# Kernel tuning notes

Measured on AMD Instinct MI355X. Metric: run time of the kernel, lower is better.

The kernel has to match this reference:

```python
import jax, jax.numpy as jnp
import numpy as np

D_MODEL = 2048
N_HEADS = 16
HEAD_DIM = D_MODEL // N_HEADS  # 128
MAX_POS = 2048


def _precompute_cos_sin(max_pos, head_dim):
    inv_freq = 1.0 / (10000.0 ** (jnp.arange(0, head_dim, 2, dtype=jnp.float32) / head_dim))
    t = jnp.arange(max_pos, dtype=jnp.float32)
    freqs = jnp.outer(t, inv_freq)          # [max_pos, head_dim//2]
    emb = jnp.concatenate([freqs, freqs], axis=-1)  # [max_pos, head_dim]
    return jnp.cos(emb), jnp.sin(emb)


def _rotate_half(x):
    x1, x2 = x[..., : x.shape[-1] // 2], x[..., x.shape[-1] // 2 :]
    return jnp.concatenate([-x2, x1], axis=-1)


def setup_inputs() -> dict:
    key = jax.random.key(0)
    kx, kq, kk, kv, ko = jax.random.split(key, 5)
    B, S = 2, 2048
    x = jax.random.normal(kx, (B, S, D_MODEL), dtype=jnp.float32)
    scale = 1.0 / np.sqrt(D_MODEL)
    # torch Linear weights are [out_features, in_features]
    Wq = jax.random.normal(kq, (D_MODEL, D_MODEL), dtype=jnp.float32) * scale
    Wk = jax.random.normal(kk, (D_MODEL, D_MODEL), dtype=jnp.float32) * scale
    Wv = jax.random.normal(kv, (D_MODEL, D_MODEL), dtype=jnp.float32) * scale
    Wo = jax.random.normal(ko, (D_MODEL, D_MODEL), dtype=jnp.float32) * scale
    cos, sin = _precompute_cos_sin(MAX_POS, HEAD_DIM)
    # causal mask: True where attention is disallowed (masked_fill semantics)
    mask = jnp.triu(jnp.ones((S, S), dtype=bool), k=1)
    mask = jnp.broadcast_to(mask[None], (B, S, S))
    return {"x": x, "Wq": Wq, "Wk": Wk, "Wv": Wv, "Wo": Wo,
            "cos": cos, "sin": sin, "mask": mask}


def reference(x, Wq, Wk, Wv, Wo, cos, sin, mask):
    B, S, _ = x.shape
    H, Dh = N_HEADS, HEAD_DIM
    scaling = Dh ** -0.5

    def split_heads(y):  # [B,S,D] -> [B,H,S,Dh]
        return y.reshape(B, S, H, Dh).transpose(0, 2, 1, 3)

    q = split_heads(x @ Wq.T)
    k = split_heads(x @ Wk.T)
    v = split_heads(x @ Wv.T)

    c = cos[:S][None, None]  # [1,1,S,Dh]
    s = sin[:S][None, None]
    q = q * c + _rotate_half(q) * s
    k = k * c + _rotate_half(k) * s

    scores = jnp.einsum("bhqd,bhkd->bhqk", q, k) * scaling
    scores = jnp.where(mask[:, None], -jnp.inf, scores)
    attn = jax.nn.softmax(scores, axis=-1)
    out = jnp.einsum("bhqk,bhkd->bhqd", attn, v)  # [B,H,S,Dh]
    out = out.transpose(0, 2, 1, 3).reshape(B, S, H * Dh)
    return out @ Wo.T
```

## Files before the change

kernel.cpp:

```cpp
#include <hip/hip_runtime.h>

typedef float f32x4 __attribute__((ext_vector_type(4)));
typedef short s16x8 __attribute__((ext_vector_type(8)));
typedef unsigned short u16;
typedef u16 u16x4 __attribute__((ext_vector_type(4)));

#define SEQ 2048
#define BATCH 2
#define NH 16
#define DH 128
#define DM 2048
#define MROWS (BATCH * SEQ)

__device__ constexpr float SCALE2 = 0.12751879523531f;

__device__ __forceinline__ u16 f2bf(float f) {
  unsigned u = __float_as_uint(f);
  u += 0x7fffu + ((u >> 16) & 1u);
  return (u16)(u >> 16);
}
__device__ __forceinline__ float bf2f(u16 b) {
  return __uint_as_float(((unsigned)b) << 16);
}

__device__ __forceinline__ void gld_lds16(const void* g, void* l) {
  __builtin_amdgcn_global_load_lds(
      (const __attribute__((address_space(1))) unsigned int*)g,
      (__attribute__((address_space(3))) unsigned int*)l, 16, 0, 0);
}

__global__ __launch_bounds__(256) void cast_all(const float* __restrict__ x,
                                                const float* __restrict__ Wq,
                                                const float* __restrict__ Wk,
                                                const float* __restrict__ Wv,
                                                const float* __restrict__ Wo,
                                                u16* __restrict__ xb,
                                                u16* __restrict__ Wqkvb,
                                                u16* __restrict__ Wob) {
  long i = (long)blockIdx.x * 256 + threadIdx.x;
  const float* src;
  u16* dst;
  long off;
  if (i < 2097152)      { src = x;  dst = xb;              off = i; }
  else if (i < 3145728) { src = Wq; dst = Wqkvb;           off = i - 2097152; }
  else if (i < 4194304) { src = Wk; dst = Wqkvb + 4194304; off = i - 3145728; }
  else if (i < 5242880) { src = Wv; dst = Wqkvb + 8388608; off = i - 4194304; }
  else                  { src = Wo; dst = Wob;             off = i - 5242880; }
  float4 v = ((const float4*)src)[off];
  u16x4 o;
  o[0] = f2bf(v.x); o[1] = f2bf(v.y); o[2] = f2bf(v.z); o[3] = f2bf(v.w);
  ((u16x4*)dst)[off] = o;
}


#define GEMM_V3_BODY(A, B, NTILE_SHIFT)                                       \
  __shared__ u16 Alds[2][256 * 64];                                           \
  __shared__ u16 Blds[2][128 * 64];                                           \
  const int tid = threadIdx.x, wave = tid >> 6, lane = tid & 63;              \
  const int r = lane & 15, g = lane >> 4;                                     \
  const int wm = wave >> 1, wn = wave & 1;                                    \
  const int bid = blockIdx.x;                                                 \
  const int swz = (bid & 7) * (gridDim.x >> 3) + (bid >> 3);                  \
  const int m0 = (swz & 15) * 256;                                            \
  const int n0 = (swz >> 4) * 128;                                            \
  const int lrow = lane >> 3;                                                 \
  const int csrc = (lane & 7) ^ lrow;                                         \
  f32x4 acc[4][4] = {};                                                       \
  s16x8 aF[2][4], bF[2][4];                                                   \
  STAGE_A(0, 0, 0); STAGE_B(0, 0, 0); STAGE_A(0, 1, 0); STAGE_B(0, 1, 0);     \
  STAGE_A(1, 0, 1); STAGE_B(1, 0, 1);                                         \
  asm volatile("s_waitcnt vmcnt(3)" ::: "memory");                            \
  __builtin_amdgcn_s_barrier();                                               \
  for (int t = 0; t < 32; ++t) {                                              \
    const int bt = t & 1, bn = bt ^ 1;                                        \
    const u16* Ab = Alds[bt];                                                 \
    const u16* Bb = Blds[bt];                                                 \
    READ_K(0);                                                                \
    __builtin_amdgcn_sched_barrier(0);                                        \
    READ_K(1);                                                                \
    if (t < 31) { STAGE_A(t + 1, 1, bn); STAGE_B(t + 1, 1, bn); }             \
    asm volatile("s_waitcnt lgkmcnt(8)" ::: "memory");                        \
    __builtin_amdgcn_sched_barrier(0);                                        \
    MFMA_K(0);                                                                \
    asm volatile("s_waitcnt lgkmcnt(0)" ::: "memory");                        \
    __builtin_amdgcn_sched_barrier(0);                                        \
    __builtin_amdgcn_s_barrier();                                             \
    if (t < 30) { STAGE_A(t + 2, 0, bt); STAGE_B(t + 2, 0, bt); }             \
    MFMA_K(1);                                                                \
    if (t < 30)       asm volatile("s_waitcnt vmcnt(3)" ::: "memory");        \
    else if (t == 30) asm volatile("s_waitcnt vmcnt(0)" ::: "memory");        \
    __builtin_amdgcn_s_barrier();                                             \
  }

#define STAGE_A(TA, MH, BUF) do {                                             \
  _Pragma("unroll") for (int i_ = 0; i_ < 2; ++i_) {                          \
    const int row0_ = (MH) * 128 + i_ * 64 + wave * 8;                        \
    gld_lds16(A + (long)(m0 + row0_ + lrow) * 2048 + (TA) * 64 + csrc * 8,    \
              &Alds[BUF][row0_ * 64]);                                        \
  } } while (0)
#define STAGE_B(TA, NHh, BUF) do {                                            \
    const int row0_ = (NHh) * 64 + wave * 8;                                  \
    gld_lds16(B + (long)(n0 + row0_ + lrow) * 2048 + (TA) * 64 + csrc * 8,    \
              &Blds[BUF][row0_ * 64]);                                        \
  } while (0)
#define READ_K(KK) do {                                                       \
  _Pragma("unroll") for (int mf = 0; mf < 4; ++mf) {                          \
    const int arow = wm * 64 + mf * 16 + r;                                   \
    aF[KK][mf] = *(const s16x8*)&Ab[arow * 64 +                               \
                                    ((((KK) * 4 + g) ^ (arow & 7)) * 8)];     \
  }                                                                           \
  _Pragma("unroll") for (int nf = 0; nf < 4; ++nf) {                          \
    const int brow = wn * 64 + nf * 16 + r;                                   \
    bF[KK][nf] = *(const s16x8*)&Bb[brow * 64 +                               \
                                    ((((KK) * 4 + g) ^ (brow & 7)) * 8)];     \
  } } while (0)
#define MFMA_K(KK) do {                                                       \
  __builtin_amdgcn_s_setprio(1);                                              \
  _Pragma("unroll") for (int mf = 0; mf < 4; ++mf)                            \
    _Pragma("unroll") for (int nf = 0; nf < 4; ++nf)                          \
      acc[mf][nf] = __builtin_amdgcn_mfma_f32_16x16x32_bf16(                  \
          aF[KK][mf], bF[KK][nf], acc[mf][nf], 0, 0, 0);                      \
  __builtin_amdgcn_s_setprio(0);                                              \
} while (0)

__global__ __launch_bounds__(512, 2) void gemm_qkv8(const u16* __restrict__ A,
                                                    const u16* __restrict__ B,
                                                    u16* __restrict__ Qo,
                                                    u16* __restrict__ Ko,
                                                    u16* __restrict__ Vo) {
  GEMM_V3_BODY(A, B, 4)
  u16* Cb = (n0 < 2048) ? Qo : (n0 < 4096 ? Ko : Vo);
  const int nc0 = n0 & 2047;
#pragma unroll
  for (int mi = 0; mi < 4; ++mi)
#pragma unroll
    for (int ni = 0; ni < 4; ++ni)
#pragma unroll
      for (int q = 0; q < 4; ++q)
        Cb[(long)(m0 + wm * 64 + mi * 16 + g * 4 + q) * 2048 +
           nc0 + wn * 64 + ni * 16 + r] = f2bf(acc[mi][ni][q]);
}

__global__ __launch_bounds__(512, 2) void gemm_wo(const u16* __restrict__ A,
                                                  const u16* __restrict__ B,
                                                  float* __restrict__ C) {
  GEMM_V3_BODY(A, B, 4)
#pragma unroll
  for (int mi = 0; mi < 4; ++mi)
#pragma unroll
    for (int ni = 0; ni < 4; ++ni)
#pragma unroll
      for (int q = 0; q < 4; ++q)
        C[(long)(m0 + wm * 64 + mi * 16 + g * 4 + q) * 2048 +
          n0 + wn * 64 + ni * 16 + r] = acc[mi][ni][q];
}

#undef MFMA_K
#undef READ_K
#undef STAGE_B
#undef STAGE_A
#undef GEMM_V3_BODY

__global__ __launch_bounds__(256) void rope_kernel(u16* __restrict__ Q, u16* __restrict__ K,
                                                   const float* __restrict__ cosT,
                                                   const float* __restrict__ sinT) {
  int idx = blockIdx.x * 256 + threadIdx.x;
  int d = idx & 63;
  int h = (idx >> 6) & 15;
  int s = (idx >> 10) & 2047;
  int b = idx >> 21;
  float c = cosT[s * DH + d];
  float sn = sinT[s * DH + d];
  long base = ((long)(b * SEQ + s)) * DM + h * DH + d;
  float q1 = bf2f(Q[base]), q2 = bf2f(Q[base + 64]);
  Q[base]      = f2bf(q1 * c - q2 * sn);
  Q[base + 64] = f2bf(q2 * c + q1 * sn);
  float k1 = bf2f(K[base]), k2 = bf2f(K[base + 64]);
  K[base]      = f2bf(k1 * c - k2 * sn);
  K[base + 64] = f2bf(k2 * c + k1 * sn);
}

__global__ __launch_bounds__(256) void transpose_v(const u16* __restrict__ Vlin,
                                                   u16* __restrict__ Vt) {
  __shared__ u16 tile[64][129];
  int t = threadIdx.x;
  int st = blockIdx.x & 31;
  int h = (blockIdx.x >> 5) & 15;
  int b = blockIdx.x >> 9;
  int s0 = st * 64;
  const u16* src = Vlin + ((long)(b * SEQ + s0)) * DM + h * DH;
#pragma unroll
  for (int rr = 0; rr < 4; rr++) {
    int row = rr * 16 + (t >> 4);
    int col = (t & 15) * 8;
    s16x8 v = *(const s16x8*)&src[(long)row * DM + col];
#pragma unroll
    for (int j = 0; j < 8; j++) tile[row][col + j] = (u16)v[j];
  }
  __syncthreads();
  u16* dst = Vt + ((long)(b * NH + h)) * DH * SEQ + s0;
#pragma unroll
  for (int rr = 0; rr < 4; rr++) {
    int d = rr * 32 + (t >> 3);
    int sc = (t & 7) * 8;
    s16x8 o;
#pragma unroll
    for (int j = 0; j < 8; j++) o[j] = (short)tile[sc + j][d];
    *(s16x8*)&dst[(long)d * SEQ + sc] = o;
  }
}


__device__ __forceinline__ void softmax_swapped(
    f32x4 (&s)[4], float& mi, float& li,
    u16 (&pl)[16][64], float (&als)[16],
    int qbase, int k0, int r, int g) {
  const int q = qbase + r;
  const bool edge = (k0 + 63) > qbase;
  float v[16];
#pragma unroll
  for (int kk = 0; kk < 4; kk++)
#pragma unroll
    for (int i = 0; i < 4; i++) {
      float x = s[kk][i] * SCALE2;
      if (edge && (k0 + kk * 16 + g * 4 + i > q)) x = -1e30f;
      v[kk * 4 + i] = x;
    }
  float t8[8], t4[4];
#pragma unroll
  for (int j = 0; j < 8; j++) t8[j] = fmaxf(v[2 * j], v[2 * j + 1]);
#pragma unroll
  for (int j = 0; j < 4; j++) t4[j] = fmaxf(t8[2 * j], t8[2 * j + 1]);
  float mx = fmaxf(fmaxf(t4[0], t4[1]), fmaxf(t4[2], t4[3]));
  mx = fmaxf(mx, __shfl_xor(mx, 16, 64));
  mx = fmaxf(mx, __shfl_xor(mx, 32, 64));
  const float mnew = fmaxf(mi, mx);
  const float a = exp2f(mi - mnew);
  float p[16];
#pragma unroll
  for (int j = 0; j < 16; j++) p[j] = exp2f(v[j] - mnew);
  float s8[8], s4[4];
#pragma unroll
  for (int j = 0; j < 8; j++) s8[j] = p[2 * j] + p[2 * j + 1];
#pragma unroll
  for (int j = 0; j < 4; j++) s4[j] = s8[2 * j] + s8[2 * j + 1];
  float ps = (s4[0] + s4[1]) + (s4[2] + s4[3]);
  ps += __shfl_xor(ps, 16, 64);
  ps += __shfl_xor(ps, 32, 64);
  li = li * a + ps;
  mi = mnew;
  const int sw = (r & 7) << 3;
#pragma unroll
  for (int kk = 0; kk < 4; kk++) {
    u16x4 w;
#pragma unroll
    for (int i = 0; i < 4; i++) w[i] = f2bf(p[kk * 4 + i]);
    *(u16x4*)&pl[r][(kk * 16 + g * 4) ^ sw] = w;
  }
  als[r] = a;
}

__global__ __launch_bounds__(512, 4) void attn_kernel(const u16* __restrict__ Q,
                                                      const u16* __restrict__ K,
                                                      const u16* __restrict__ Vt,
                                                      u16* __restrict__ O) {
  __shared__ u16 Klds[64 * 128];
  __shared__ u16 Vlds[128 * 64];
  __shared__ u16 Plds[8][16][64];
  __shared__ float Alds[8][16];

  const int tid = threadIdx.x, wave = tid >> 6, lane = tid & 63;
  const int r = lane & 15, g = lane >> 4;
  const int bh = blockIdx.x & 31;
  const int jj = blockIdx.x >> 5;
  const int j = (jj < 8) ? jj : 23 - jj;
  const int h = bh & 15, b = bh >> 4;
  const bool isB = wave >= 4;
  const int w4 = wave & 3;
  const int strip = isB ? (31 - j) : j;
  const int q0 = strip * 64 + w4 * 16;
  const int nt = 32 - j;
  const int lastA = j;

  const u16* Qbh = Q + (long)b * SEQ * DM + h * DH;
  const u16* Kbh = K + (long)b * SEQ * DM + h * DH;
  const u16* Vbh = Vt + ((long)(b * NH + h)) * DH * SEQ;

  s16x8 qf[4];
#pragma unroll
  for (int jq = 0; jq < 4; jq++)
    qf[jq] = *(const s16x8*)&Qbh[(long)(q0 + r) * DM + jq * 32 + g * 8];

  f32x4 oacc[8] = {};
  float mi = -1e30f, li = 0.f;

  for (int kt = 0; kt < nt; ++kt) {
    const int k0 = kt * 64;
    __syncthreads();
#pragma unroll
    for (int c = 0; c < 2; ++c) {
      const int s = c * 512 + tid;
      const int krow = s >> 4;
      const int kch = (s & 15) ^ (krow & 7);
      gld_lds16(Kbh + (long)(k0 + krow) * DM + kch * 8,
                &Klds[(c * 512 + wave * 64) * 8]);
      const int vrow = s >> 3;
      const int vch = (s & 7) ^ (vrow & 7);
      gld_lds16(Vbh + (long)vrow * SEQ + k0 + vch * 8,
                &Vlds[(c * 512 + wave * 64) * 8]);
    }
    __syncthreads();

    const bool active = isB || (kt <= lastA);
    if (active) {
      f32x4 sacc[4] = {};
#pragma unroll
      for (int kk = 0; kk < 4; kk++) {
#pragma unroll
        for (int jq = 0; jq < 4; jq++) {
          s16x8 kf = *(const s16x8*)&Klds[(kk * 16 + r) * 128 +
                                          (((jq * 4 + g) ^ (r & 7)) * 8)];
          sacc[kk] = __builtin_amdgcn_mfma_f32_16x16x32_bf16(kf, qf[jq], sacc[kk], 0, 0, 0);
        }
      }
      softmax_swapped(sacc, mi, li, Plds[wave], Alds[wave], q0, k0, r, g);

      f32x4 av = *(const f32x4*)&Alds[wave][g * 4];
#pragma unroll
      for (int f = 0; f < 8; f++)
#pragma unroll
        for (int i = 0; i < 4; i++) oacc[f][i] *= av[i];

      const int sw = (r & 7) << 3;
#pragma unroll
      for (int kc = 0; kc < 2; kc++) {
        s16x8 pf = *(const s16x8*)&Plds[wave][r][(kc * 32 + g * 8) ^ sw];
#pragma unroll
        for (int f = 0; f < 8; f++) {
          s16x8 vf = *(const s16x8*)&Vlds[(f * 16 + r) * 64 +
                                          (((kc * 4 + g) ^ (r & 7)) * 8)];
          oacc[f] = __builtin_amdgcn_mfma_f32_16x16x32_bf16(pf, vf, oacc[f], 0, 0, 0);
        }
      }
    }
  }

  Alds[wave][r] = 1.f / li;
  f32x4 iv = *(const f32x4*)&Alds[wave][g * 4];
  u16* Obh = O + (long)b * SEQ * DM + h * DH;
#pragma unroll
  for (int f = 0; f < 8; f++)
#pragma unroll
    for (int i = 0; i < 4; i++)
      Obh[(long)(q0 + g * 4 + i) * DM + f * 16 + r] = f2bf(oacc[f][i] * iv[i]);
}

extern "C" void kernel_launch(void* const* d_in, const int* in_sizes, int n_in,
                              void* d_out, int out_size, void* d_ws, size_t ws_size,
                              hipStream_t stream) {
  const float* x    = (const float*)d_in[0];
  const float* Wq   = (const float*)d_in[1];
  const float* Wk   = (const float*)d_in[2];
  const float* Wv   = (const float*)d_in[3];
  const float* Wo   = (const float*)d_in[4];
  const float* cosT = (const float*)d_in[5];
  const float* sinT = (const float*)d_in[6];

  if (ws_size < (size_t)134217728) return;

  char* ws = (char*)d_ws;
  u16* xb    = (u16*)(ws);
  u16* Wqkvb = (u16*)(ws + 16777216);
  u16* Wob   = (u16*)(ws + 41943040);
  u16* Qlin  = (u16*)(ws + 50331648);
  u16* Klin  = (u16*)(ws + 67108864);
  u16* Vlin  = (u16*)(ws + 83886080);
  u16* Vt    = (u16*)(ws + 100663296);
  u16* Olin  = (u16*)(ws + 117440512);

  cast_all<<<24576, 256, 0, stream>>>(x, Wq, Wk, Wv, Wo, xb, Wqkvb, Wob);

  gemm_qkv8<<<768, 512, 0, stream>>>(xb, Wqkvb, Qlin, Klin, Vlin);

  rope_kernel<<<16384, 256, 0, stream>>>(Qlin, Klin, cosT, sinT);
  transpose_v<<<1024, 256, 0, stream>>>(Vlin, Vt);
  attn_kernel<<<512, 512, 0, stream>>>(Qlin, Klin, Vt, Olin);

  gemm_wo<<<256, 512, 0, stream>>>(Olin, Wob, (float*)d_out);
}
```

Before: 264.9 us.

## Fuse V transpose into QKV GEMM epilogue and give attention waves two query tiles

The QKV GEMM epilogue for V tiles now stages results in shared memory and writes them directly in transposed [b,h,d,s] layout, which removes the separate transpose_v kernel and the Vlin round trip. The attention kernel drops from 8 waves per block to 4, and each wave now processes two 16-row query tiles. This reuses each K and V fragment read from LDS across twice as many MFMAs. The trade-offs are fewer waves to hide latency, higher register pressure from doubled accumulators, and extra shared-memory synchronization in the GEMM epilogue.

```diff
diff --git a/kernel.cpp b/kernel.cpp
--- a/kernel.cpp
+++ b/kernel.cpp
@@ -53,7 +53,7 @@
 }
 
 
-#define GEMM_V3_BODY(A, B, NTILE_SHIFT)                                       \
+#define GEMM_V3_BODY(A, B)                                                    \
   __shared__ u16 Alds[2][256 * 64];                                           \
   __shared__ u16 Blds[2][128 * 64];                                           \
   const int tid = threadIdx.x, wave = tid >> 6, lane = tid & 63;              \
@@ -127,24 +127,50 @@
                                                     const u16* __restrict__ B,
                                                     u16* __restrict__ Qo,
                                                     u16* __restrict__ Ko,
-                                                    u16* __restrict__ Vo) {
-  GEMM_V3_BODY(A, B, 4)
-  u16* Cb = (n0 < 2048) ? Qo : (n0 < 4096 ? Ko : Vo);
-  const int nc0 = n0 & 2047;
-#pragma unroll
-  for (int mi = 0; mi < 4; ++mi)
-#pragma unroll
-    for (int ni = 0; ni < 4; ++ni)
-#pragma unroll
-      for (int q = 0; q < 4; ++q)
-        Cb[(long)(m0 + wm * 64 + mi * 16 + g * 4 + q) * 2048 +
-           nc0 + wn * 64 + ni * 16 + r] = f2bf(acc[mi][ni][q]);
+                                                    u16* __restrict__ Vt) {
+  GEMM_V3_BODY(A, B)
+  if (n0 < 4096) {
+    u16* Cb = (n0 < 2048) ? Qo : Ko;
+    const int nc0 = n0 & 2047;
+#pragma unroll
+    for (int mi = 0; mi < 4; ++mi)
+#pragma unroll
+      for (int ni = 0; ni < 4; ++ni)
+#pragma unroll
+        for (int q = 0; q < 4; ++q)
+          Cb[(long)(m0 + wm * 64 + mi * 16 + g * 4 + q) * 2048 +
+             nc0 + wn * 64 + ni * 16 + r] = f2bf(acc[mi][ni][q]);
+  } else {
+    u16* T = (u16*)Alds;
+#pragma unroll
+    for (int mi = 0; mi < 4; ++mi)
+#pragma unroll
+      for (int ni = 0; ni < 4; ++ni) {
+        const int d = wn * 64 + ni * 16 + r;
+        const int sb = wm * 64 + mi * 16 + g * 4;
+        u16x4 w;
+#pragma unroll
+        for (int q = 0; q < 4; ++q) w[q] = f2bf(acc[mi][ni][q]);
+        *(u16x4*)&T[d * 256 + (((sb >> 3) ^ (d & 7)) << 3) + (sb & 7)] = w;
+      }
+    __syncthreads();
+    const int b_ = m0 >> 11, s0l = m0 & 2047;
+    const int hh = (n0 - 4096) >> 7;
+    const int dd = tid >> 2, part = tid & 3;
+    u16* vrow = Vt + ((long)((b_ * 16 + hh) * 128 + dd)) * 2048 + s0l;
+#pragma unroll
+    for (int cc = 0; cc < 8; ++cc) {
+      const int chunk = cc * 4 + part;
+      s16x8 v = *(const s16x8*)&T[dd * 256 + ((chunk ^ (dd & 7)) << 3)];
+      *(s16x8*)&vrow[chunk * 8] = v;
+    }
+  }
 }
 
 __global__ __launch_bounds__(512, 2) void gemm_wo(const u16* __restrict__ A,
                                                   const u16* __restrict__ B,
                                                   float* __restrict__ C) {
-  GEMM_V3_BODY(A, B, 4)
+  GEMM_V3_BODY(A, B)
 #pragma unroll
   for (int mi = 0; mi < 4; ++mi)
 #pragma unroll
@@ -180,36 +206,6 @@
   K[base + 64] = f2bf(k2 * c + k1 * sn);
 }
 
-__global__ __launch_bounds__(256) void transpose_v(const u16* __restrict__ Vlin,
-                                                   u16* __restrict__ Vt) {
-  __shared__ u16 tile[64][129];
-  int t = threadIdx.x;
-  int st = blockIdx.x & 31;
-  int h = (blockIdx.x >> 5) & 15;
-  int b = blockIdx.x >> 9;
-  int s0 = st * 64;
-  const u16* src = Vlin + ((long)(b * SEQ + s0)) * DM + h * DH;
-#pragma unroll
-  for (int rr = 0; rr < 4; rr++) {
-    int row = rr * 16 + (t >> 4);
-    int col = (t & 15) * 8;
-    s16x8 v = *(const s16x8*)&src[(long)row * DM + col];
-#pragma unroll
-    for (int j = 0; j < 8; j++) tile[row][col + j] = (u16)v[j];
-  }
-  __syncthreads();
-  u16* dst = Vt + ((long)(b * NH + h)) * DH * SEQ + s0;
-#pragma unroll
-  for (int rr = 0; rr < 4; rr++) {
-    int d = rr * 32 + (t >> 3);
-    int sc = (t & 7) * 8;
-    s16x8 o;
-#pragma unroll
-    for (int j = 0; j < 8; j++) o[j] = (short)tile[sc + j][d];
-    *(s16x8*)&dst[(long)d * SEQ + sc] = o;
-  }
-}
-
 
 __device__ __forceinline__ void softmax_swapped(
     f32x4 (&s)[4], float& mi, float& li,
@@ -260,14 +256,14 @@
   als[r] = a;
 }
 
-__global__ __launch_bounds__(512, 4) void attn_kernel(const u16* __restrict__ Q,
+__global__ __launch_bounds__(256, 2) void attn_kernel(const u16* __restrict__ Q,
                                                       const u16* __restrict__ K,
                                                       const u16* __restrict__ Vt,
                                                       u16* __restrict__ O) {
   __shared__ u16 Klds[64 * 128];
   __shared__ u16 Vlds[128 * 64];
-  __shared__ u16 Plds[8][16][64];
-  __shared__ float Alds[8][16];
+  __shared__ u16 Plds[4][2][16][64];
+  __shared__ float Alds[4][2][16];
 
   const int tid = threadIdx.x, wave = tid >> 6, lane = tid & 63;
   const int r = lane & 15, g = lane >> 4;
@@ -275,10 +271,10 @@
   const int jj = blockIdx.x >> 5;
   const int j = (jj < 8) ? jj : 23 - jj;
   const int h = bh & 15, b = bh >> 4;
-  const bool isB = wave >= 4;
-  const int w4 = wave & 3;
+  const bool isB = wave >= 2;
+  const int w2 = wave & 1;
   const int strip = isB ? (31 - j) : j;
-  const int q0 = strip * 64 + w4 * 16;
+  const int q0 = strip * 64 + w2 * 32;
   const int nt = 32 - j;
   const int lastA = j;
 
@@ -286,73 +282,87 @@
   const u16* Kbh = K + (long)b * SEQ * DM + h * DH;
   const u16* Vbh = Vt + ((long)(b * NH + h)) * DH * SEQ;
 
-  s16x8 qf[4];
-#pragma unroll
-  for (int jq = 0; jq < 4; jq++)
-    qf[jq] = *(const s16x8*)&Qbh[(long)(q0 + r) * DM + jq * 32 + g * 8];
-
-  f32x4 oacc[8] = {};
-  float mi = -1e30f, li = 0.f;
+  s16x8 qfA[4], qfB[4];
+#pragma unroll
+  for (int jq = 0; jq < 4; jq++) {
+    qfA[jq] = *(const s16x8*)&Qbh[(long)(q0 + r) * DM + jq * 32 + g * 8];
+    qfB[jq] = *(const s16x8*)&Qbh[(long)(q0 + 16 + r) * DM + jq * 32 + g * 8];
+  }
+
+  f32x4 oaccA[8] = {}, oaccB[8] = {};
+  float miA = -1e30f, liA = 0.f, miB = -1e30f, liB = 0.f;
 
   for (int kt = 0; kt < nt; ++kt) {
     const int k0 = kt * 64;
     __syncthreads();
 #pragma unroll
-    for (int c = 0; c < 2; ++c) {
-      const int s = c * 512 + tid;
+    for (int c = 0; c < 4; ++c) {
+      const int s = c * 256 + tid;
       const int krow = s >> 4;
       const int kch = (s & 15) ^ (krow & 7);
       gld_lds16(Kbh + (long)(k0 + krow) * DM + kch * 8,
-                &Klds[(c * 512 + wave * 64) * 8]);
+                &Klds[(c * 256 + wave * 64) * 8]);
       const int vrow = s >> 3;
       const int vch = (s & 7) ^ (vrow & 7);
       gld_lds16(Vbh + (long)vrow * SEQ + k0 + vch * 8,
-                &Vlds[(c * 512 + wave * 64) * 8]);
+                &Vlds[(c * 256 + wave * 64) * 8]);
     }
     __syncthreads();
 
     const bool active = isB || (kt <= lastA);
     if (active) {
-      f32x4 sacc[4] = {};
+      f32x4 sA[4] = {}, sB[4] = {};
 #pragma unroll
       for (int kk = 0; kk < 4; kk++) {
 #pragma unroll
         for (int jq = 0; jq < 4; jq++) {
           s16x8 kf = *(const s16x8*)&Klds[(kk * 16 + r) * 128 +
                                           (((jq * 4 + g) ^ (r & 7)) * 8)];
-          sacc[kk] = __builtin_amdgcn_mfma_f32_16x16x32_bf16(kf, qf[jq], sacc[kk], 0, 0, 0);
+          sA[kk] = __builtin_amdgcn_mfma_f32_16x16x32_bf16(kf, qfA[jq], sA[kk], 0, 0, 0);
+          sB[kk] = __builtin_amdgcn_mfma_f32_16x16x32_bf16(kf, qfB[jq], sB[kk], 0, 0, 0);
         }
       }
-      softmax_swapped(sacc, mi, li, Plds[wave], Alds[wave], q0, k0, r, g);
-
-      f32x4 av = *(const f32x4*)&Alds[wave][g * 4];
+      softmax_swapped(sA, miA, liA, Plds[wave][0], Alds[wave][0], q0, k0, r, g);
+      softmax_swapped(sB, miB, liB, Plds[wave][1], Alds[wave][1], q0 + 16, k0, r, g);
+
+      f32x4 avA = *(const f32x4*)&Alds[wave][0][g * 4];
+      f32x4 avB = *(const f32x4*)&Alds[wave][1][g * 4];
 #pragma unroll
       for (int f = 0; f < 8; f++)
 #pragma unroll
-        for (int i = 0; i < 4; i++) oacc[f][i] *= av[i];
+        for (int i = 0; i < 4; i++) {
+          oaccA[f][i] *= avA[i];
+          oaccB[f][i] *= avB[i];
+        }
 
       const int sw = (r & 7) << 3;
 #pragma unroll
       for (int kc = 0; kc < 2; kc++) {
-        s16x8 pf = *(const s16x8*)&Plds[wave][r][(kc * 32 + g * 8) ^ sw];
+        s16x8 pfA = *(const s16x8*)&Plds[wave][0][r][(kc * 32 + g * 8) ^ sw];
+        s16x8 pfB = *(const s16x8*)&Plds[wave][1][r][(kc * 32 + g * 8) ^ sw];
 #pragma unroll
         for (int f = 0; f < 8; f++) {
           s16x8 vf = *(const s16x8*)&Vlds[(f * 16 + r) * 64 +
                                           (((kc * 4 + g) ^ (r & 7)) * 8)];
-          oacc[f] = __builtin_amdgcn_mfma_f32_16x16x32_bf16(pf, vf, oacc[f], 0, 0, 0);
+          oaccA[f] = __builtin_amdgcn_mfma_f32_16x16x32_bf16(pfA, vf, oaccA[f], 0, 0, 0);
+          oaccB[f] = __builtin_amdgcn_mfma_f32_16x16x32_bf16(pfB, vf, oaccB[f], 0, 0, 0);
         }
       }
     }
   }
 
-  Alds[wave][r] = 1.f / li;
-  f32x4 iv = *(const f32x4*)&Alds[wave][g * 4];
+  Alds[wave][0][r] = 1.f / liA;
+  Alds[wave][1][r] = 1.f / liB;
+  f32x4 ivA = *(const f32x4*)&Alds[wave][0][g * 4];
+  f32x4 ivB = *(const f32x4*)&Alds[wave][1][g * 4];
   u16* Obh = O + (long)b * SEQ * DM + h * DH;
 #pragma unroll
   for (int f = 0; f < 8; f++)
 #pragma unroll
-    for (int i = 0; i < 4; i++)
-      Obh[(long)(q0 + g * 4 + i) * DM + f * 16 + r] = f2bf(oacc[f][i] * iv[i]);
+    for (int i = 0; i < 4; i++) {
+      Obh[(long)(q0 + g * 4 + i) * DM + f * 16 + r] = f2bf(oaccA[f][i] * ivA[i]);
+      Obh[(long)(q0 + 16 + g * 4 + i) * DM + f * 16 + r] = f2bf(oaccB[f][i] * ivB[i]);
+    }
 }
 
 extern "C" void kernel_launch(void* const* d_in, const int* in_sizes, int n_in,
@@ -374,17 +384,15 @@
   u16* Wob   = (u16*)(ws + 41943040);
   u16* Qlin  = (u16*)(ws + 50331648);
   u16* Klin  = (u16*)(ws + 67108864);
-  u16* Vlin  = (u16*)(ws + 83886080);
   u16* Vt    = (u16*)(ws + 100663296);
   u16* Olin  = (u16*)(ws + 117440512);
 
   cast_all<<<24576, 256, 0, stream>>>(x, Wq, Wk, Wv, Wo, xb, Wqkvb, Wob);
 
-  gemm_qkv8<<<768, 512, 0, stream>>>(xb, Wqkvb, Qlin, Klin, Vlin);
+  gemm_qkv8<<<768, 512, 0, stream>>>(xb, Wqkvb, Qlin, Klin, Vt);
 
   rope_kernel<<<16384, 256, 0, stream>>>(Qlin, Klin, cosT, sinT);
-  transpose_v<<<1024, 256, 0, stream>>>(Vlin, Vt);
-  attn_kernel<<<512, 512, 0, stream>>>(Qlin, Klin, Vt, Olin);
+  attn_kernel<<<512, 256, 0, stream>>>(Qlin, Klin, Vt, Olin);
 
   gemm_wo<<<256, 512, 0, stream>>>(Olin, Wob, (float*)d_out);
 }
```

Result: slower. 270.9 us (+2.3%).

## Fuse RoPE and V transpose into QKV GEMM epilogue via LDS staging

Applied to the files above, without the earlier changes.

The QKV GEMM epilogue now stages each output tile through shared memory. For Q and K tiles it applies rotary embedding using the partner half-dimension before writing. For V tiles it writes directly in the transposed per-head layout the attention kernel expects. This removes the separate rope and transpose kernels along with their extra global read/write passes, at the cost of an extra LDS round trip, a barrier and per-element cos/sin loads in the GEMM epilogue.

```diff
diff --git a/kernel.cpp b/kernel.cpp
--- a/kernel.cpp
+++ b/kernel.cpp
@@ -53,9 +53,10 @@
 }
 
 
-#define GEMM_V3_BODY(A, B, NTILE_SHIFT)                                       \
-  __shared__ u16 Alds[2][256 * 64];                                           \
-  __shared__ u16 Blds[2][128 * 64];                                           \
+#define GEMM_V3_BODY(A, B)                                                    \
+  __shared__ u16 SMEM[49152];                                      \
+  u16 (*Alds)[16384] = (u16(*)[16384])SMEM;                    \
+  u16 (*Blds)[8192]  = (u16(*)[8192])(SMEM + 32768);           \
   const int tid = threadIdx.x, wave = tid >> 6, lane = tid & 63;              \
   const int r = lane & 15, g = lane >> 4;                                     \
   const int wm = wave >> 1, wn = wave & 1;                                    \
@@ -125,26 +126,76 @@
 
 __global__ __launch_bounds__(512, 2) void gemm_qkv8(const u16* __restrict__ A,
                                                     const u16* __restrict__ B,
+                                                    const float* __restrict__ cosT,
+                                                    const float* __restrict__ sinT,
                                                     u16* __restrict__ Qo,
                                                     u16* __restrict__ Ko,
-                                                    u16* __restrict__ Vo) {
-  GEMM_V3_BODY(A, B, 4)
-  u16* Cb = (n0 < 2048) ? Qo : (n0 < 4096 ? Ko : Vo);
-  const int nc0 = n0 & 2047;
-#pragma unroll
-  for (int mi = 0; mi < 4; ++mi)
-#pragma unroll
-    for (int ni = 0; ni < 4; ++ni)
-#pragma unroll
-      for (int q = 0; q < 4; ++q)
-        Cb[(long)(m0 + wm * 64 + mi * 16 + g * 4 + q) * 2048 +
-           nc0 + wn * 64 + ni * 16 + r] = f2bf(acc[mi][ni][q]);
+                                                    u16* __restrict__ Vt) {
+  GEMM_V3_BODY(A, B)
+  if (n0 < 4096) {
+    u16* T = SMEM;
+#pragma unroll
+    for (int mi = 0; mi < 4; ++mi)
+#pragma unroll
+      for (int ni = 0; ni < 4; ++ni) {
+        const int rl = wm * 64 + mi * 16 + g * 4;
+        const int dh = wn * 64 + ni * 16 + r;
+#pragma unroll
+        for (int q = 0; q < 4; ++q)
+          T[(rl + q) * 136 + dh] = f2bf(acc[mi][ni][q]);
+      }
+    __syncthreads();
+    u16* Cb = (n0 < 2048) ? Qo : Ko;
+    const int nc0 = n0 & 2047;
+    const float sgn = wn ? 1.f : -1.f;
+#pragma unroll
+    for (int mi = 0; mi < 4; ++mi)
+#pragma unroll
+      for (int ni = 0; ni < 4; ++ni) {
+        const int rl = wm * 64 + mi * 16 + g * 4;
+        const int dh = wn * 64 + ni * 16 + r;
+#pragma unroll
+        for (int q = 0; q < 4; ++q) {
+          const int row = m0 + rl + q;
+          const int spos = row & 2047;
+          const float c  = cosT[spos * 128 + dh];
+          const float sn = sinT[spos * 128 + dh];
+          const float v = bf2f(T[(rl + q) * 136 + dh]);
+          const float p = bf2f(T[(rl + q) * 136 + (dh ^ 64)]);
+          Cb[(long)row * 2048 + nc0 + dh] = f2bf(v * c + sgn * p * sn);
+        }
+      }
+  } else {
+    u16* T = SMEM;
+#pragma unroll
+    for (int mi = 0; mi < 4; ++mi)
+#pragma unroll
+      for (int ni = 0; ni < 4; ++ni) {
+        const int d = wn * 64 + ni * 16 + r;
+        const int sb = wm * 64 + mi * 16 + g * 4;
+        u16x4 w;
+#pragma unroll
+        for (int q = 0; q < 4; ++q) w[q] = f2bf(acc[mi][ni][q]);
+        *(u16x4*)&T[d * 256 + (((sb >> 3) ^ (d & 7)) << 3) + (sb & 7)] = w;
+      }
+    __syncthreads();
+    const int b_ = m0 >> 11, s0l = m0 & 2047;
+    const int hh = (n0 - 4096) >> 7;
+    const int dd = tid >> 2, part = tid & 3;
+    u16* vrow = Vt + ((long)((b_ * 16 + hh) * 128 + dd)) * 2048 + s0l;
+#pragma unroll
+    for (int cc = 0; cc < 8; ++cc) {
+      const int chunk = cc * 4 + part;
+      s16x8 v = *(const s16x8*)&T[dd * 256 + ((chunk ^ (dd & 7)) << 3)];
+      *(s16x8*)&vrow[chunk * 8] = v;
+    }
+  }
 }
 
 __global__ __launch_bounds__(512, 2) void gemm_wo(const u16* __restrict__ A,
                                                   const u16* __restrict__ B,
                                                   float* __restrict__ C) {
-  GEMM_V3_BODY(A, B, 4)
+  GEMM_V3_BODY(A, B)
 #pragma unroll
   for (int mi = 0; mi < 4; ++mi)
 #pragma unroll
@@ -160,55 +211,6 @@
 #undef STAGE_B
 #undef STAGE_A
 #undef GEMM_V3_BODY
-
-__global__ __launch_bounds__(256) void rope_kernel(u16* __restrict__ Q, u16* __restrict__ K,
-                                                   const float* __restrict__ cosT,
-                                                   const float* __restrict__ sinT) {
-  int idx = blockIdx.x * 256 + threadIdx.x;
-  int d = idx & 63;
-  int h = (idx >> 6) & 15;
-  int s = (idx >> 10) & 2047;
-  int b = idx >> 21;
-  float c = cosT[s * DH + d];
-  float sn = sinT[s * DH + d];
-  long base = ((long)(b * SEQ + s)) * DM + h * DH + d;
-  float q1 = bf2f(Q[base]), q2 = bf2f(Q[base + 64]);
-  Q[base]      = f2bf(q1 * c - q2 * sn);
-  Q[base + 64] = f2bf(q2 * c + q1 * sn);
-  float k1 = bf2f(K[base]), k2 = bf2f(K[base + 64]);
-  K[base]      = f2bf(k1 * c - k2 * sn);
-  K[base + 64] = f2bf(k2 * c + k1 * sn);
-}
-
-__global__ __launch_bounds__(256) void transpose_v(const u16* __restrict__ Vlin,
-                                                   u16* __restrict__ Vt) {
-  __shared__ u16 tile[64][129];
-  int t = threadIdx.x;
-  int st = blockIdx.x & 31;
-  int h = (blockIdx.x >> 5) & 15;
-  int b = blockIdx.x >> 9;
-  int s0 = st * 64;
-  const u16* src = Vlin + ((long)(b * SEQ + s0)) * DM + h * DH;
-#pragma unroll
-  for (int rr = 0; rr < 4; rr++) {
-    int row = rr * 16 + (t >> 4);
-    int col = (t & 15) * 8;
-    s16x8 v = *(const s16x8*)&src[(long)row * DM + col];
-#pragma unroll
-    for (int j = 0; j < 8; j++) tile[row][col + j] = (u16)v[j];
-  }
-  __syncthreads();
-  u16* dst = Vt + ((long)(b * NH + h)) * DH * SEQ + s0;
-#pragma unroll
-  for (int rr = 0; rr < 4; rr++) {
-    int d = rr * 32 + (t >> 3);
-    int sc = (t & 7) * 8;
-    s16x8 o;
-#pragma unroll
-    for (int j = 0; j < 8; j++) o[j] = (short)tile[sc + j][d];
-    *(s16x8*)&dst[(long)d * SEQ + sc] = o;
-  }
-}
 
 
 __device__ __forceinline__ void softmax_swapped(
@@ -374,16 +376,13 @@
   u16* Wob   = (u16*)(ws + 41943040);
   u16* Qlin  = (u16*)(ws + 50331648);
   u16* Klin  = (u16*)(ws + 67108864);
-  u16* Vlin  = (u16*)(ws + 83886080);
   u16* Vt    = (u16*)(ws + 100663296);
   u16* Olin  = (u16*)(ws + 117440512);
 
   cast_all<<<24576, 256, 0, stream>>>(x, Wq, Wk, Wv, Wo, xb, Wqkvb, Wob);
 
-  gemm_qkv8<<<768, 512, 0, stream>>>(xb, Wqkvb, Qlin, Klin, Vlin);
-
-  rope_kernel<<<16384, 256, 0, stream>>>(Qlin, Klin, cosT, sinT);
-  transpose_v<<<1024, 256, 0, stream>>>(Vlin, Vt);
+  gemm_qkv8<<<768, 512, 0, stream>>>(xb, Wqkvb, cosT, sinT, Qlin, Klin, Vt);
+
   attn_kernel<<<512, 512, 0, stream>>>(Qlin, Klin, Vt, Olin);
 
   gemm_wo<<<256, 512, 0, stream>>>(Olin, Wob, (float*)d_out);
```

Result: faster. 255.4 us (-3.6%).
